# Performance work log

Hardware: AMD Instinct MI355X
Metric: run time of the kernel (lower is better)

## Reference

```python
import jax, jax.numpy as jnp
import numpy as np
import math

# Model hyperparameters (match init_kwargs)
B, S, E = 8, 1024, 512
NUM_HEADS = 8
NQ = 16        # n_qubits for quantum attention
NQF = 16       # n_qubits_ffn for quantum feed-forward
FFN = 2048
L = 4          # num_layers
EPS = 1e-5


def _sinusoidal_pe(seq_len, embed_dim):
    pos = np.arange(seq_len)[:, None].astype(np.float32)
    div = np.exp(np.arange(0, embed_dim, 2).astype(np.float32) * (-math.log(10000.0) / embed_dim))
    pe = np.zeros((seq_len, embed_dim), dtype=np.float32)
    pe[:, 0::2] = np.sin(pos * div)
    pe[:, 1::2] = np.cos(pos * div)
    return jnp.asarray(pe)


def setup_inputs() -> dict:
    key = jax.random.key(0)
    ks = jax.random.split(key, 12)
    x = jax.random.normal(ks[0], (B, S, E), dtype=jnp.float32)
    pe = _sinusoidal_pe(S, E)
    # per-layer parameters stacked along leading L axis
    theta_attn = jax.random.normal(ks[1], (L, NQ), dtype=jnp.float32) * 0.1   # RY angles (attention circuit)
    theta_ffn = jax.random.normal(ks[2], (L, NQF), dtype=jnp.float32) * 0.1    # RY angles (ffn circuit)
    W_combine = jax.random.normal(ks[3], (L, E, NQ), dtype=jnp.float32) / math.sqrt(NQ)
    W1 = jax.random.normal(ks[4], (L, FFN, NQF), dtype=jnp.float32) / math.sqrt(NQF)
    W2 = jax.random.normal(ks[5], (L, E, FFN), dtype=jnp.float32) / math.sqrt(FFN)
    g1 = jnp.ones((L, E), dtype=jnp.float32)
    b1 = jnp.zeros((L, E), dtype=jnp.float32)
    g2 = jnp.ones((L, E), dtype=jnp.float32)
    b2 = jnp.zeros((L, E), dtype=jnp.float32)
    return {"x": x, "pe": pe, "theta_attn": theta_attn, "theta_ffn": theta_ffn,
            "W_combine": W_combine, "W1": W1, "W2": W2,
            "g1": g1, "b1": b1, "g2": g2, "b2": b2}


def _layer_norm(h, g, b):
    m = jnp.mean(h, axis=-1, keepdims=True)
    v = jnp.var(h, axis=-1, keepdims=True)
    return (h - m) * jax.lax.rsqrt(v + EPS) * g + b


def _quantum_features(h, theta, n_qubits):
    # Each wire: |0> -> RX(x_i) -> RY(theta_i) -> <Z_i> = cos(theta_i) * cos(x_i)
    # Product state => exact closed form; vectorizes the per-token circuit loop.
    return jnp.cos(theta)[None, None, :] * jnp.cos(h[..., :n_qubits])


def reference(x, pe, theta_attn, theta_ffn, W_combine, W1, W2, g1, b1, g2, b2):
    b_, s_, e_ = x.shape
    dk = NQ // NUM_HEADS
    h = x + pe[None, :s_, :]
    for l in range(L):
        qv = _quantum_features(h, theta_attn[l], NQ)                 # [B,S,NQ]
        q = qv.reshape(b_, s_, NUM_HEADS, dk).transpose(0, 2, 1, 3)  # [B,H,S,dk]
        scores = jnp.einsum('bhqd,bhkd->bhqk', q, q) / math.sqrt(dk)
        probs = jax.nn.softmax(scores, axis=-1)
        attn = jnp.einsum('bhqk,bhkd->bhqd', probs, q)               # [B,H,S,dk]
        attn = attn.transpose(0, 2, 1, 3).reshape(b_, s_, NQ)
        attn_out = attn @ W_combine[l].T                             # [B,S,E]
        h = _layer_norm(h + attn_out, g1[l], b1[l])
        # --- quantum feed-forward ---
        qf = _quantum_features(h, theta_ffn[l], NQF)                 # [B,S,NQF]
        ffn_out = jax.nn.relu(qf @ W1[l].T) @ W2[l].T                # [B,S,E]
        h = _layer_norm(h + ffn_out, g2[l], b2[l])
    return h
```

## Files before the change

kernel.cpp:

```cpp
#include <hip/hip_runtime.h>
#include <cstdint>
#include <cstddef>

#define BB 8
#define SS 1024
#define EE 512
#define NQB 16
#define FF 2048

typedef unsigned short u16;
typedef __attribute__((ext_vector_type(8))) short short8;
typedef __attribute__((ext_vector_type(4))) float f32x4;

#define FLAG_OFF   0
#define H16_OFF    4096
#define QF_OFF     528384
#define W1P_OFF    1052672
#define STATS_OFF  1314816
#define H_OFF      2097152
#define W2P_OFF    18874368

__device__ __forceinline__ float u2f(u16 u){ return __uint_as_float(((unsigned)u)<<16); }
__device__ __forceinline__ u16 f2bf(float x){
  unsigned u = __float_as_uint(x);
  u += 0x7FFF + ((u>>16)&1);
  return (u16)(u>>16);
}
__device__ __forceinline__ float ldg(const void* p,int f,size_t i){
  return f ? ((const float*)p)[i] : u2f(((const u16*)p)[i]);
}
__device__ __forceinline__ float4 ldg4(const void* p,int f,size_t i){
  float4 r;
  if (f){ r = ((const float4*)p)[i>>2]; }
  else { ushort4 v = ((const ushort4*)p)[i>>2];
         r.x=u2f(v.x); r.y=u2f(v.y); r.z=u2f(v.z); r.w=u2f(v.w); }
  return r;
}
__device__ __forceinline__ short8 ldfrag8(const void* p,int f,size_t i){
  short8 r;
  if (f){
    float4 A  = ((const float4*)p)[i>>2];
    float4 Bv = ((const float4*)p)[(i>>2)+1];
    r[0]=(short)f2bf(A.x);  r[1]=(short)f2bf(A.y);  r[2]=(short)f2bf(A.z);  r[3]=(short)f2bf(A.w);
    r[4]=(short)f2bf(Bv.x); r[5]=(short)f2bf(Bv.y); r[6]=(short)f2bf(Bv.z); r[7]=(short)f2bf(Bv.w);
  } else {
    r = *(const short8*)((const u16*)p + i);
  }
  return r;
}
__device__ __forceinline__ void tok_stats(const float* st, int tok, float& m, float& rs){
  float S1 = 0.f, S2 = 0.f;
  #pragma unroll
  for (int nb=0; nb<4; ++nb){
    float2 p = *(const float2*)&st[((size_t)tok*4+nb)*2];
    S1 += p.x; S2 += p.y;
  }
  m = S1*(1.f/512.f);
  float var = S2*(1.f/512.f) - m*m;
  rs = rsqrtf(var + 1e-5f);
}

__global__ void detect_k(const u16* __restrict__ x, int* __restrict__ flag){
  __shared__ int cnt;
  if (threadIdx.x==0) cnt=0;
  __syncthreads();
  int c=0;
  for (int i=threadIdx.x;i<4096;i+=256){
    u16 v = x[(size_t)i*2];
    int ex = (v>>7)&0xFF;
    c += (ex>=160) ? 1 : 0;
  }
  atomicAdd(&cnt,c);
  __syncthreads();
  if (threadIdx.x==0) *flag = (cnt>64) ? 1 : 0;
}

__global__ __launch_bounds__(256) void w1pack_k(const void* __restrict__ W1,
    const void* __restrict__ thf, u16* __restrict__ W1p, const int* __restrict__ flag){
  int f = *flag;
  int idx = blockIdx.x*256 + threadIdx.x;
  int l = idx>>12, nt = (idx>>5)&127, lane32 = idx&31;
  int quad = lane32>>4, col = lane32&15;
  short8 v = ldfrag8(W1, f, ((size_t)l*FF + nt*16 + col)*16 + quad*8);
  short8 o;
  #pragma unroll
  for (int j=0;j<8;++j){
    float th = ldg(thf, f, (size_t)l*16 + quad*8 + j);
    o[j] = (short)f2bf(__cosf(th) * u2f((u16)v[j]));
  }
  *(short8*)(W1p + (size_t)idx*8) = o;
}

__global__ __launch_bounds__(256) void w2pack_k(const void* __restrict__ W2,
    u16* __restrict__ W2p, const int* __restrict__ flag){
  int f = *flag;
  int idx = blockIdx.x*256 + threadIdx.x;
  int lane = idx&63, kb = (idx>>6)&63, teg = (idx>>12)&31, l = idx>>17;
  int quad = lane>>4, col = lane&15;
  short8 v = ldfrag8(W2, f, ((size_t)l*EE + teg*16 + col)*FF + kb*32 + quad*8);
  *(short8*)(W2p + (size_t)idx*8) = v;
}

__global__ __launch_bounds__(256) void add_pe_k(const void* __restrict__ x,
    const void* __restrict__ pe, float* __restrict__ hw, const int* __restrict__ flag){
  int f = *flag;
  size_t e = ((size_t)blockIdx.x*256 + threadIdx.x)*4;
  float4 xv = ldg4(x,f,e);
  float4 pv = ldg4(pe,f,e & (size_t)(SS*EE-1));
  float4 o; o.x=xv.x+pv.x; o.y=xv.y+pv.y; o.z=xv.z+pv.z; o.w=xv.w+pv.w;
  *(float4*)&hw[e] = o;
}

__global__ __launch_bounds__(512) void attn_comb_k(float* __restrict__ hw,
    const void* __restrict__ thA, const void* __restrict__ Wc,
    const void* __restrict__ g1v, const void* __restrict__ b1v,
    const void* __restrict__ g2v, const void* __restrict__ b2v,
    const float* __restrict__ st, float* __restrict__ h16,
    float* __restrict__ qf, const int* __restrict__ flag, int lazy, int l){
  __shared__ float SM2[20544];
  float* qq2  = SM2;
  float* part = SM2 + 16384;
  float* msK  = SM2 + 17920;
  float* AFR  = SM2 + 19968;
  float* MS   = SM2 + 20480;
  float* RS   = SM2 + 20512;
  float* outC = SM2;
  int f = *flag;
  int tid = threadIdx.x;
  int b = blockIdx.x>>5, grp = blockIdx.x&31;
  size_t bbase = (size_t)b*SS*EE;
  int tok0 = b*SS + grp*32;

  if (lazy){
    #pragma unroll
    for (int t2=0;t2<2;++t2){
      int j = tid*2+t2;
      float m, rs; tok_stats(st, b*SS+j, m, rs);
      msK[j*2]=m; msK[j*2+1]=rs;
    }
  }
  __syncthreads();
  {
    int jl = tid>>2, d0 = (tid&3)*4;
    int h0 = d0>>1;
    float ct[4], gl2[4]={1,1,1,1}, bl2[4]={0,0,0,0};
    #pragma unroll
    for (int d=0;d<4;++d) ct[d] = __cosf(ldg(thA,f,(size_t)l*16+d0+d));
    if (lazy){
      float4 gv = ldg4(g2v,f,(size_t)(l-1)*EE+d0);
      float4 bv = ldg4(b2v,f,(size_t)(l-1)*EE+d0);
      gl2[0]=gv.x; gl2[1]=gv.y; gl2[2]=gv.z; gl2[3]=gv.w;
      bl2[0]=bv.x; bl2[1]=bv.y; bl2[2]=bv.z; bl2[3]=bv.w;
    }
    #pragma unroll 2
    for (int it=0; it<8; ++it){
      int j = jl + it*128;
      float4 hv = *(const float4*)&hw[bbase + (size_t)j*EE + d0];
      float vv[4] = {hv.x, hv.y, hv.z, hv.w};
      if (lazy){
        float m = msK[j*2], rs = msK[j*2+1];
        #pragma unroll
        for (int d=0;d<4;++d) vv[d] = fmaf((vv[d]-m)*rs, gl2[d], bl2[d]);
      }
      float2 o0, o1;
      o0.x = ct[0]*__cosf(vv[0]); o0.y = ct[1]*__cosf(vv[1]);
      o1.x = ct[2]*__cosf(vv[2]); o1.y = ct[3]*__cosf(vv[3]);
      *(float2*)&qq2[h0*2048 + j*2]     = o0;
      *(float2*)&qq2[(h0+1)*2048 + j*2] = o1;
    }
  }
  __syncthreads();
  {
    int r = tid&31, hd = (tid>>5)&7, kz = tid>>8;
    int rg = grp*32 + r;
    const float* qh = &qq2[hd*2048];
    float a0 = qh[rg*2], a1 = qh[rg*2+1];
    const float sc = 0.70710678118f;
    float a0s = a0*sc, a1s = a1*sc;
    float dA=0.f, x0A=0.f, x1A=0.f, dB=0.f, x0B=0.f, x1B=0.f;
    const float* qp = qh + kz*1024;
    for (int j=0; j<512; j+=4){
      float4 P = *(const float4*)(qp + j*2);
      float4 Q = *(const float4*)(qp + j*2 + 4);
      float e0 = __expf(fmaf(a1s,P.y, a0s*P.x));
      float e1 = __expf(fmaf(a1s,P.w, a0s*P.z));
      float e2 = __expf(fmaf(a1s,Q.y, a0s*Q.x));
      float e3 = __expf(fmaf(a1s,Q.w, a0s*Q.z));
      dA += e0; x0A = fmaf(e0,P.x,x0A); x1A = fmaf(e0,P.y,x1A);
      dB += e1; x0B = fmaf(e1,P.z,x0B); x1B = fmaf(e1,P.w,x1B);
      dA += e2; x0A = fmaf(e2,Q.x,x0A); x1A = fmaf(e2,Q.y,x1A);
      dB += e3; x0B = fmaf(e3,Q.z,x0B); x1B = fmaf(e3,Q.w,x1B);
    }
    float* pp = &part[((r*8+hd)*2+kz)*3];
    pp[0]=dA+dB; pp[1]=x0A+x0B; pp[2]=x1A+x1B;
  }
  __syncthreads();
  if (tid < 256){
    int r = tid&31, hd = tid>>5;
    const float* p0 = &part[((r*8+hd)*2+0)*3];
    const float* p1 = &part[((r*8+hd)*2+1)*3];
    float d = p0[0]+p1[0];
    float inv = 1.f/d;
    AFR[r*16 + 2*hd]   = (p0[1]+p1[1])*inv;
    AFR[r*16 + 2*hd+1] = (p0[2]+p1[2])*inv;
  }
  __syncthreads();
  {
    int e0 = tid;
    float wc[16];
    size_t wb = (size_t)l*EE*16 + (size_t)e0*16;
    #pragma unroll
    for (int q4=0;q4<4;++q4){
      float4 a = ldg4(Wc,f, wb + q4*4);
      wc[q4*4+0]=a.x; wc[q4*4+1]=a.y; wc[q4*4+2]=a.z; wc[q4*4+3]=a.w;
    }
    float gl0=1.f,bl0=0.f;
    if (lazy){
      gl0 = ldg(g2v,f,(size_t)(l-1)*EE+e0);
      bl0 = ldg(b2v,f,(size_t)(l-1)*EE+e0);
    }
    for (int t=0; t<32; ++t){
      float v0 = hw[(size_t)(tok0+t)*EE + e0];
      if (lazy){
        float m = msK[(grp*32+t)*2], rs = msK[(grp*32+t)*2+1];
        v0 = fmaf((v0-m)*rs, gl0, bl0);
      }
      float s0 = v0;
      #pragma unroll
      for (int q4=0;q4<4;++q4){
        float4 av = *(const float4*)&AFR[t*16 + q4*4];
        s0 = fmaf(av.x, wc[q4*4+0], fmaf(av.y, wc[q4*4+1], fmaf(av.z, wc[q4*4+2], fmaf(av.w, wc[q4*4+3], s0))));
      }
      outC[t*520 + e0] = s0;
    }
  }
  __syncthreads();
  {
    int token = tid>>4, prt = tid&15;
    float s=0.f, s2=0.f;
    #pragma unroll 8
    for (int i2=0;i2<32;++i2){
      float vv = outC[token*520 + prt + 16*i2];
      s += vv; s2 = fmaf(vv,vv,s2);
    }
    #pragma unroll
    for (int off=8; off; off>>=1){ s += __shfl_down(s,off,16); s2 += __shfl_down(s2,off,16); }
    if (prt==0){
      float m = s*(1.f/512.f);
      float var = s2*(1.f/512.f) - m*m;
      MS[token] = m; RS[token] = rsqrtf(var+1e-5f);
    }
  }
  __syncthreads();
  for (int u=tid; u<32*128; u+=512){
    int tok = u>>7, c4 = (u&127)*4;
    float4 vv = *(const float4*)&outC[tok*520 + c4];
    float m = MS[tok], rs = RS[tok];
    float4 gv = ldg4(g1v,f,(size_t)l*EE + c4);
    float4 bv = ldg4(b1v,f,(size_t)l*EE + c4);
    float4 o;
    o.x = fmaf((vv.x-m)*rs, gv.x, bv.x);
    o.y = fmaf((vv.y-m)*rs, gv.y, bv.y);
    o.z = fmaf((vv.z-m)*rs, gv.z, bv.z);
    o.w = fmaf((vv.w-m)*rs, gv.w, bv.w);
    if (c4 >= 16){
      *(float4*)&hw[(size_t)(tok0+tok)*EE + c4] = o;
    } else {
      *(float4*)&h16[(size_t)(tok0+tok)*16 + c4] = o;
      float4 qo;
      qo.x=__cosf(o.x); qo.y=__cosf(o.y); qo.z=__cosf(o.z); qo.w=__cosf(o.w);
      *(float4*)&qf[(size_t)(tok0+tok)*16 + c4] = qo;
    }
  }
}

__global__ __launch_bounds__(256) void ffn5_k(float* __restrict__ hw,
    const float* __restrict__ h16, const float* __restrict__ qf,
    const u16* __restrict__ W1p, const void* __restrict__ W2,
    const u16* __restrict__ W2p, float* __restrict__ st,
    const int* __restrict__ flag, int cv, int l){
  __shared__ float SMF[8448];
  u16* HtA = (u16*)SMF;
  float* outL = SMF;

  int f = *flag;
  int tid = threadIdx.x, w = tid>>6, lane = tid&63;
  int quad = lane>>4, col = lane&15;
  int mb = blockIdx.x, nb = blockIdx.y;
  int tok0 = mb*64;

  short8 a0[4];
  #pragma unroll
  for (int mt=0; mt<4; ++mt){
    short8 z = {0,0,0,0,0,0,0,0};
    if (quad < 2){
      const float* qp = qf + (size_t)(tok0 + mt*16 + col)*16 + quad*8;
      float4 A = *(const float4*)qp, B = *(const float4*)(qp+4);
      z[0]=(short)f2bf(A.x); z[1]=(short)f2bf(A.y); z[2]=(short)f2bf(A.z); z[3]=(short)f2bf(A.w);
      z[4]=(short)f2bf(B.x); z[5]=(short)f2bf(B.y); z[6]=(short)f2bf(B.z); z[7]=(short)f2bf(B.w);
    }
    a0[mt] = z;
  }

  f32x4 acc[4][2];
  #pragma unroll
  for (int i=0;i<4;++i){ acc[i][0]=(f32x4){0,0,0,0}; acc[i][1]=(f32x4){0,0,0,0}; }
  const f32x4 zc = {0.f,0.f,0.f,0.f};
  size_t w2base = (size_t)l*EE*FF;

  auto loadW1 = [&](int k0)->short8{
    short8 z = {0,0,0,0,0,0,0,0};
    if (quad < 2)
      z = *(const short8*)(W1p + (((size_t)l*128 + (k0>>4) + w)*32 + quad*16 + col)*8);
    return z;
  };
  auto loadB2 = [&](short8 (&B)[2][2], int k0){
    if (cv){
      #pragma unroll
      for (int et=0;et<2;++et)
        #pragma unroll
        for (int s=0;s<2;++s)
          B[et][s] = *(const short8*)(W2p + ((((size_t)l*32 + nb*8 + w*2 + et)*64)
                       + (k0>>5) + s)*512 + lane*8);
    } else {
      #pragma unroll
      for (int et=0;et<2;++et)
        #pragma unroll
        for (int s=0;s<2;++s)
          B[et][s] = ldfrag8(W2, f, w2base
                       + (size_t)(nb*128 + w*32 + et*16 + col)*FF + k0 + s*32 + quad*8);
    }
  };
  auto gemm1 = [&](int buf, short8 b1){
    int kl = w*16 + quad*4;
    int s  = kl>>5, q2 = (kl&31)>>3, j0 = kl&7;
    u16* dst0 = &HtA[buf*4096 + s*512 + (q2*16+col)*8 + j0];
    #pragma unroll
    for (int mt=0; mt<4; ++mt){
      f32x4 hc = __builtin_amdgcn_mfma_f32_16x16x32_bf16(b1, a0[mt], zc, 0,0,0);
      ushort4 pk;
      pk.x = f2bf(fmaxf(hc[0],0.f)); pk.y = f2bf(fmaxf(hc[1],0.f));
      pk.z = f2bf(fmaxf(hc[2],0.f)); pk.w = f2bf(fmaxf(hc[3],0.f));
      *(ushort4*)(dst0 + mt*1024) = pk;
    }
  };

  short8 B2c[2][2], B2n[2][2];
  short8 b1n;
  {
    short8 b1 = loadW1(0);
    loadB2(B2c, 0);
    gemm1(0, b1);
    b1n = loadW1(64);
  }
  __syncthreads();
  for (int i=0; i<32; ++i){
    if (i < 31){
      loadB2(B2n, (i+1)*64);
      gemm1((i+1)&1, b1n);
      int k2 = (i+2 < 32) ? (i+2)*64 : 0;
      b1n = loadW1(k2);
    }
    int cb = i&1;
    #pragma unroll
    for (int s=0;s<2;++s){
      short8 A2[4];
      #pragma unroll
      for (int mt=0;mt<4;++mt)
        A2[mt] = *(const short8*)&HtA[cb*4096 + (mt*2+s)*512 + lane*8];
      #pragma unroll
      for (int et=0;et<2;++et)
        #pragma unroll
        for (int mt=0;mt<4;++mt)
          acc[mt][et] = __builtin_amdgcn_mfma_f32_16x16x32_bf16(A2[mt], B2c[et][s], acc[mt][et], 0,0,0);
    }
    __syncthreads();
    if (i < 31){
      #pragma unroll
      for (int et=0;et<2;++et){ B2c[et][0]=B2n[et][0]; B2c[et][1]=B2n[et][1]; }
    }
  }

  #pragma unroll
  for (int mt=0; mt<4; ++mt){
    #pragma unroll
    for (int r=0;r<4;++r){
      int ltok = mt*16 + quad*4 + r;
      size_t hb = (size_t)(tok0+ltok)*EE + nb*128;
      #pragma unroll
      for (int et=0;et<2;++et){
        int eloc = w*32 + et*16 + col;
        int eg = nb*128 + eloc;
        float rsd = (eg < 16) ? h16[(size_t)(tok0+ltok)*16 + eg] : hw[hb + eloc];
        outL[ltok*132 + eloc] = acc[mt][et][r] + rsd;
      }
    }
  }
  __syncthreads();
  {
    int token = tid>>2, prt = tid&3;
    float s=0.f, s2=0.f;
    #pragma unroll 8
    for (int i2=0;i2<32;++i2){
      float vv = outL[token*132 + prt + 4*i2];
      s += vv; s2 = fmaf(vv,vv,s2);
    }
    s += __shfl_down(s,2,4); s2 += __shfl_down(s2,2,4);
    s += __shfl_down(s,1,4); s2 += __shfl_down(s2,1,4);
    if (prt==0){
      float2 o; o.x = s; o.y = s2;
      *(float2*)&st[((size_t)(tok0+token)*4 + nb)*2] = o;
    }
  }
  for (int u=tid; u<64*32; u+=256){
    int tok = u>>5, c4 = (u&31)*4;
    float4 vv = *(const float4*)&outL[tok*132 + c4];
    *(float4*)&hw[(size_t)(tok0+tok)*EE + nb*128 + c4] = vv;
  }
}

__global__ __launch_bounds__(256) void conv2_k(const float* __restrict__ hw,
    const float* __restrict__ st, const void* __restrict__ g2v,
    const void* __restrict__ b2v, void* __restrict__ out,
    const int* __restrict__ flag){
  int f = *flag;
  size_t i = (size_t)blockIdx.x*256 + threadIdx.x;
  int tok = (int)(i>>7), c4 = ((int)i&127)*4;
  float4 v = *(const float4*)&hw[i*4];
  float m, rs; tok_stats(st, tok, m, rs);
  float4 gv = ldg4(g2v,f,(size_t)3*EE + c4);
  float4 bv = ldg4(b2v,f,(size_t)3*EE + c4);
  float4 o;
  o.x = fmaf((v.x-m)*rs, gv.x, bv.x);
  o.y = fmaf((v.y-m)*rs, gv.y, bv.y);
  o.z = fmaf((v.z-m)*rs, gv.z, bv.z);
  o.w = fmaf((v.w-m)*rs, gv.w, bv.w);
  if (f){
    *(float4*)((float*)out + i*4) = o;
  } else {
    ushort4 ob; ob.x=f2bf(o.x); ob.y=f2bf(o.y); ob.z=f2bf(o.z); ob.w=f2bf(o.w);
    *(ushort4*)((u16*)out + i*4) = ob;
  }
}

extern "C" void kernel_launch(void* const* d_in, const int* in_sizes, int n_in,
                              void* d_out, int out_size, void* d_ws, size_t ws_size,
                              hipStream_t stream) {
  (void)in_sizes; (void)n_in; (void)out_size;
  char* ws = (char*)d_ws;
  int*   flag = (int*)(ws + FLAG_OFF);
  float* h16  = (float*)(ws + H16_OFF);
  float* qf   = (float*)(ws + QF_OFF);
  u16*   w1p  = (u16*)(ws + W1P_OFF);
  float* st   = (float*)(ws + STATS_OFF);
  float* hw   = (float*)(ws + H_OFF);
  u16*   w2p  = (u16*)(ws + W2P_OFF);
  int cv = (ws_size >= (size_t)W2P_OFF + ((size_t)8<<20)) ? 1 : 0;

  detect_k<<<1,256,0,stream>>>((const u16*)d_in[0], flag);
  w1pack_k<<<64,256,0,stream>>>(d_in[5], d_in[3], w1p, flag);
  if (cv) w2pack_k<<<2048,256,0,stream>>>(d_in[6], w2p, flag);
  add_pe_k<<<4096,256,0,stream>>>(d_in[0], d_in[1], hw, flag);
  for (int l=0; l<4; ++l){
    int lazy = (l>0) ? 1 : 0;
    attn_comb_k<<<256,512,0,stream>>>(hw, d_in[2], d_in[4], d_in[7], d_in[8],
                                      d_in[9], d_in[10], st, h16, qf,
                                      flag, lazy, l);
    ffn5_k<<<dim3(128,4),256,0,stream>>>(hw, h16, qf, w1p, d_in[6], w2p,
                                         st, flag, cv, l);
  }
  conv2_k<<<4096,256,0,stream>>>(hw, st, d_in[9], d_in[10], d_out, flag);
}
```

Before: 399.6 us.

## Halve attention tokens per block and double FFN K-step per pipeline stage

```diff
diff --git a/kernel.cpp b/kernel.cpp
--- a/kernel.cpp
+++ b/kernel.cpp
@@ -117,19 +117,19 @@
     const void* __restrict__ g2v, const void* __restrict__ b2v,
     const float* __restrict__ st, float* __restrict__ h16,
     float* __restrict__ qf, const int* __restrict__ flag, int lazy, int l){
-  __shared__ float SM2[20544];
+  __shared__ float SM2[20256];
   float* qq2  = SM2;
   float* part = SM2 + 16384;
   float* msK  = SM2 + 17920;
   float* AFR  = SM2 + 19968;
-  float* MS   = SM2 + 20480;
-  float* RS   = SM2 + 20512;
+  float* MS   = SM2 + 20224;
+  float* RS   = SM2 + 20240;
   float* outC = SM2;
   int f = *flag;
   int tid = threadIdx.x;
-  int b = blockIdx.x>>5, grp = blockIdx.x&31;
+  int b = blockIdx.x>>6, grp = blockIdx.x&63;
   size_t bbase = (size_t)b*SS*EE;
-  int tok0 = b*SS + grp*32;
+  int tok0 = b*SS + grp*16;
 
   if (lazy){
     #pragma unroll
@@ -138,8 +138,8 @@
       float m, rs; tok_stats(st, b*SS+j, m, rs);
       msK[j*2]=m; msK[j*2+1]=rs;
     }
-  }
-  __syncthreads();
+    __syncthreads();
+  }
   {
     int jl = tid>>2, d0 = (tid&3)*4;
     int h0 = d0>>1;
@@ -171,15 +171,15 @@
   }
   __syncthreads();
   {
-    int r = tid&31, hd = (tid>>5)&7, kz = tid>>8;
-    int rg = grp*32 + r;
+    int r = tid&15, hd = (tid>>4)&7, kz = tid>>7;
+    int rg = grp*16 + r;
     const float* qh = &qq2[hd*2048];
     float a0 = qh[rg*2], a1 = qh[rg*2+1];
     const float sc = 0.70710678118f;
     float a0s = a0*sc, a1s = a1*sc;
     float dA=0.f, x0A=0.f, x1A=0.f, dB=0.f, x0B=0.f, x1B=0.f;
-    const float* qp = qh + kz*1024;
-    for (int j=0; j<512; j+=4){
+    const float* qp = qh + kz*512;
+    for (int j=0; j<256; j+=4){
       float4 P = *(const float4*)(qp + j*2);
       float4 Q = *(const float4*)(qp + j*2 + 4);
       float e0 = __expf(fmaf(a1s,P.y, a0s*P.x));
@@ -191,18 +191,21 @@
       dA += e2; x0A = fmaf(e2,Q.x,x0A); x1A = fmaf(e2,Q.y,x1A);
       dB += e3; x0B = fmaf(e3,Q.z,x0B); x1B = fmaf(e3,Q.w,x1B);
     }
-    float* pp = &part[((r*8+hd)*2+kz)*3];
+    float* pp = &part[((r*8+hd)*4+kz)*3];
     pp[0]=dA+dB; pp[1]=x0A+x0B; pp[2]=x1A+x1B;
   }
   __syncthreads();
-  if (tid < 256){
-    int r = tid&31, hd = tid>>5;
-    const float* p0 = &part[((r*8+hd)*2+0)*3];
-    const float* p1 = &part[((r*8+hd)*2+1)*3];
-    float d = p0[0]+p1[0];
+  if (tid < 128){
+    int r = tid&15, hd = tid>>4;
+    float d=0.f, s0=0.f, s1=0.f;
+    #pragma unroll
+    for (int k=0;k<4;++k){
+      const float* pp = &part[((r*8+hd)*4+k)*3];
+      d += pp[0]; s0 += pp[1]; s1 += pp[2];
+    }
     float inv = 1.f/d;
-    AFR[r*16 + 2*hd]   = (p0[1]+p1[1])*inv;
-    AFR[r*16 + 2*hd+1] = (p0[2]+p1[2])*inv;
+    AFR[r*16 + 2*hd]   = s0*inv;
+    AFR[r*16 + 2*hd+1] = s1*inv;
   }
   __syncthreads();
   {
@@ -219,10 +222,11 @@
       gl0 = ldg(g2v,f,(size_t)(l-1)*EE+e0);
       bl0 = ldg(b2v,f,(size_t)(l-1)*EE+e0);
     }
-    for (int t=0; t<32; ++t){
+    #pragma unroll 4
+    for (int t=0; t<16; ++t){
       float v0 = hw[(size_t)(tok0+t)*EE + e0];
       if (lazy){
-        float m = msK[(grp*32+t)*2], rs = msK[(grp*32+t)*2+1];
+        float m = msK[(grp*16+t)*2], rs = msK[(grp*16+t)*2+1];
         v0 = fmaf((v0-m)*rs, gl0, bl0);
       }
       float s0 = v0;
@@ -236,15 +240,15 @@
   }
   __syncthreads();
   {
-    int token = tid>>4, prt = tid&15;
+    int token = tid>>5, prt = tid&31;
     float s=0.f, s2=0.f;
     #pragma unroll 8
-    for (int i2=0;i2<32;++i2){
-      float vv = outC[token*520 + prt + 16*i2];
+    for (int i2=0;i2<16;++i2){
+      float vv = outC[token*520 + prt + 32*i2];
       s += vv; s2 = fmaf(vv,vv,s2);
     }
     #pragma unroll
-    for (int off=8; off; off>>=1){ s += __shfl_down(s,off,16); s2 += __shfl_down(s2,off,16); }
+    for (int off=16; off; off>>=1){ s += __shfl_down(s,off,32); s2 += __shfl_down(s2,off,32); }
     if (prt==0){
       float m = s*(1.f/512.f);
       float var = s2*(1.f/512.f) - m*m;
@@ -252,7 +256,7 @@
     }
   }
   __syncthreads();
-  for (int u=tid; u<32*128; u+=512){
+  for (int u=tid; u<16*128; u+=512){
     int tok = u>>7, c4 = (u&127)*4;
     float4 vv = *(const float4*)&outC[tok*520 + c4];
     float m = MS[tok], rs = RS[tok];
@@ -274,12 +278,12 @@
   }
 }
 
-__global__ __launch_bounds__(256) void ffn5_k(float* __restrict__ hw,
+__global__ __launch_bounds__(256) void ffn6_k(float* __restrict__ hw,
     const float* __restrict__ h16, const float* __restrict__ qf,
     const u16* __restrict__ W1p, const void* __restrict__ W2,
     const u16* __restrict__ W2p, float* __restrict__ st,
     const int* __restrict__ flag, int cv, int l){
-  __shared__ float SMF[8448];
+  __shared__ float SMF[8704];
   u16* HtA = (u16*)SMF;
   float* outL = SMF;
 
@@ -308,76 +312,80 @@
   const f32x4 zc = {0.f,0.f,0.f,0.f};
   size_t w2base = (size_t)l*EE*FF;
 
-  auto loadW1 = [&](int k0)->short8{
+  auto loadW1 = [&](int k0, short8& A, short8& B){
     short8 z = {0,0,0,0,0,0,0,0};
-    if (quad < 2)
-      z = *(const short8*)(W1p + (((size_t)l*128 + (k0>>4) + w)*32 + quad*16 + col)*8);
-    return z;
+    A = z; B = z;
+    if (quad < 2){
+      size_t base = ((size_t)l*128 + (k0>>4) + 2*w)*32 + quad*16 + col;
+      A = *(const short8*)(W1p + base*8);
+      B = *(const short8*)(W1p + (base+32)*8);
+    }
   };
-  auto loadB2 = [&](short8 (&B)[2][2], int k0){
+  auto loadB2 = [&](short8 (&B)[2][4], int k0){
     if (cv){
       #pragma unroll
       for (int et=0;et<2;++et)
         #pragma unroll
-        for (int s=0;s<2;++s)
-          B[et][s] = *(const short8*)(W2p + ((((size_t)l*32 + nb*8 + w*2 + et)*64)
-                       + (k0>>5) + s)*512 + lane*8);
+        for (int kk=0;kk<4;++kk)
+          B[et][kk] = *(const short8*)(W2p +
+            (((size_t)l*32 + nb*8 + w*2 + et)*64 + (k0>>5) + kk)*512 + lane*8);
     } else {
       #pragma unroll
       for (int et=0;et<2;++et)
         #pragma unroll
-        for (int s=0;s<2;++s)
-          B[et][s] = ldfrag8(W2, f, w2base
-                       + (size_t)(nb*128 + w*32 + et*16 + col)*FF + k0 + s*32 + quad*8);
+        for (int kk=0;kk<4;++kk)
+          B[et][kk] = ldfrag8(W2, f, w2base
+            + (size_t)(nb*128 + (w*2+et)*16 + col)*FF + k0 + kk*32 + quad*8);
     }
   };
-  auto gemm1 = [&](int buf, short8 b1){
-    int kl = w*16 + quad*4;
-    int s  = kl>>5, q2 = (kl&31)>>3, j0 = kl&7;
-    u16* dst0 = &HtA[buf*4096 + s*512 + (q2*16+col)*8 + j0];
-    #pragma unroll
-    for (int mt=0; mt<4; ++mt){
-      f32x4 hc = __builtin_amdgcn_mfma_f32_16x16x32_bf16(b1, a0[mt], zc, 0,0,0);
-      ushort4 pk;
-      pk.x = f2bf(fmaxf(hc[0],0.f)); pk.y = f2bf(fmaxf(hc[1],0.f));
-      pk.z = f2bf(fmaxf(hc[2],0.f)); pk.w = f2bf(fmaxf(hc[3],0.f));
-      *(ushort4*)(dst0 + mt*1024) = pk;
+  auto gemm1pair = [&](int buf, short8 b1a, short8 b1b){
+    #pragma unroll
+    for (int cc=0; cc<2; ++cc){
+      short8 b1 = cc ? b1b : b1a;
+      int p = cc*16 + quad*4;
+      u16* dst = &HtA[(size_t)(buf*16 + w)*512 + ((p>>3)*16 + col)*8 + (p&7)];
+      #pragma unroll
+      for (int mt=0; mt<4; ++mt){
+        f32x4 hc = __builtin_amdgcn_mfma_f32_16x16x32_bf16(b1, a0[mt], zc, 0,0,0);
+        ushort4 pk;
+        pk.x = f2bf(fmaxf(hc[0],0.f)); pk.y = f2bf(fmaxf(hc[1],0.f));
+        pk.z = f2bf(fmaxf(hc[2],0.f)); pk.w = f2bf(fmaxf(hc[3],0.f));
+        *(ushort4*)(dst + (size_t)mt*4*512) = pk;
+      }
     }
   };
 
-  short8 B2c[2][2], B2n[2][2];
-  short8 b1n;
-  {
-    short8 b1 = loadW1(0);
-    loadB2(B2c, 0);
-    gemm1(0, b1);
-    b1n = loadW1(64);
-  }
-  __syncthreads();
-  for (int i=0; i<32; ++i){
-    if (i < 31){
-      loadB2(B2n, (i+1)*64);
-      gemm1((i+1)&1, b1n);
-      int k2 = (i+2 < 32) ? (i+2)*64 : 0;
-      b1n = loadW1(k2);
+  short8 B2c[2][4], B2n[2][4], w1a, w1b, w1na, w1nb;
+  loadB2(B2c, 0);
+  loadW1(0, w1a, w1b);
+  gemm1pair(0, w1a, w1b);
+  loadW1(128, w1na, w1nb);
+  __syncthreads();
+  for (int i=0; i<16; ++i){
+    if (i < 15){
+      loadB2(B2n, (i+1)*128);
+      gemm1pair((i+1)&1, w1na, w1nb);
+      if (i < 14) loadW1((i+2)*128, w1na, w1nb);
     }
     int cb = i&1;
     #pragma unroll
-    for (int s=0;s<2;++s){
+    for (int kk=0;kk<4;++kk){
       short8 A2[4];
       #pragma unroll
       for (int mt=0;mt<4;++mt)
-        A2[mt] = *(const short8*)&HtA[cb*4096 + (mt*2+s)*512 + lane*8];
+        A2[mt] = *(const short8*)&HtA[(size_t)(cb*16 + mt*4 + kk)*512 + lane*8];
       #pragma unroll
       for (int et=0;et<2;++et)
         #pragma unroll
         for (int mt=0;mt<4;++mt)
-          acc[mt][et] = __builtin_amdgcn_mfma_f32_16x16x32_bf16(A2[mt], B2c[et][s], acc[mt][et], 0,0,0);
+          acc[mt][et] = __builtin_amdgcn_mfma_f32_16x16x32_bf16(A2[mt], B2c[et][kk], acc[mt][et], 0,0,0);
     }
     __syncthreads();
-    if (i < 31){
-      #pragma unroll
-      for (int et=0;et<2;++et){ B2c[et][0]=B2n[et][0]; B2c[et][1]=B2n[et][1]; }
+    if (i < 15){
+      #pragma unroll
+      for (int et=0;et<2;++et)
+        #pragma unroll
+        for (int kk=0;kk<4;++kk) B2c[et][kk]=B2n[et][kk];
     }
   }
 
@@ -463,10 +471,10 @@
   add_pe_k<<<4096,256,0,stream>>>(d_in[0], d_in[1], hw, flag);
   for (int l=0; l<4; ++l){
     int lazy = (l>0) ? 1 : 0;
-    attn_comb_k<<<256,512,0,stream>>>(hw, d_in[2], d_in[4], d_in[7], d_in[8],
+    attn_comb_k<<<512,512,0,stream>>>(hw, d_in[2], d_in[4], d_in[7], d_in[8],
                                       d_in[9], d_in[10], st, h16, qf,
                                       flag, lazy, l);
-    ffn5_k<<<dim3(128,4),256,0,stream>>>(hw, h16, qf, w1p, d_in[6], w2p,
+    ffn6_k<<<dim3(128,4),256,0,stream>>>(hw, h16, qf, w1p, d_in[6], w2p,
                                          st, flag, cv, l);
   }
   conv2_k<<<4096,256,0,stream>>>(hw, st, d_in[9], d_in[10], d_out, flag);
```

Measured after the change: 370.0 us. -7.4%, faster.
